# Kernel optimization log

Hardware: AMD Instinct MI355X
Metric: run time of the kernel (lower is better)

The kernel has to match this reference:

```python
import jax, jax.numpy as jnp
import numpy as np

EPS = 1e-8  # torch CosineSimilarity default eps


def setup_inputs() -> dict:
    key = jax.random.key(0)
    ks = jax.random.split(key, 7)
    B, C, W, E, D = 64, 256, 256, 2048, 2048
    return {
        "x_img_dense": jax.random.normal(ks[0], (B, C, E), dtype=jnp.float32),
        "x_txt_dense": jax.random.normal(ks[1], (B, W, E), dtype=jnp.float32),
        "y_what_card_leader_choose": jax.random.normal(ks[2], (B, C), dtype=jnp.float32),
        "W_img1": jax.random.normal(ks[3], (D, E), dtype=jnp.float32) * 0.02,
        "b_img1": jax.random.normal(ks[4], (D,), dtype=jnp.float32) * 0.02,
        "W_words1": jax.random.normal(ks[5], (D, E), dtype=jnp.float32) * 0.02,
        "b_words1": jax.random.normal(ks[6], (D,), dtype=jnp.float32) * 0.02,
    }


def reference(x_img_dense, x_txt_dense, y_what_card_leader_choose,
              W_img1, b_img1, W_words1, b_words1):
    # Default path: img_layer=True, words_layer=True, comb_layer=False,
    # same_img_words_layer=False, gumbel=False, inference=False.
    xi = jnp.einsum('bce,de->bcd', x_img_dense, W_img1) + b_img1   # [B, C, D]
    xt = jnp.einsum('bwe,de->bwd', x_txt_dense, W_words1) + b_words1  # [B, W, D]

    # gather leader card embedding per batch element
    idx = jnp.argmax(y_what_card_leader_choose, axis=1)            # [B]
    leader = jnp.take_along_axis(xi, idx[:, None, None], axis=1)[:, 0, :]  # [B, D]

    # cosine similarity (dim=2 in torch): leader broadcast over words axis
    dot = jnp.einsum('bd,bwd->bw', leader, xt)                     # [B, W]
    denom = jnp.linalg.norm(leader, axis=-1, keepdims=True) * jnp.linalg.norm(xt, axis=-1)
    logits = dot / jnp.maximum(denom, EPS)                         # [B, W]

    # module returns softmax of `logits` (logits_final is dead code)
    return jax.nn.softmax(logits, axis=1)
```

## Files before the change

kernel.cpp:

```cpp
#include <hip/hip_runtime.h>
#include <hip/hip_bf16.h>
#include <stdint.h>

typedef unsigned short u16;
typedef __bf16 bf16x8 __attribute__((ext_vector_type(8)));
typedef float  f32x4  __attribute__((ext_vector_type(4)));
typedef float  fvec4  __attribute__((ext_vector_type(4)));

constexpr int NB = 64;
constexpr int NC = 256;
constexpr int NW = 256;
constexpr int NE = 2048;
constexpr int ND = 2048;
constexpr int MROWS = NB * NW;

constexpr int BM = 128, BN = 128, BK = 64;
constexpr int KSPLIT = 4;
constexpr int KSLICE = NE / KSPLIT;
constexpr int NSLOT = 16;

constexpr size_t OFF_IDX  = 0;
constexpr size_t OFF_PART = 256;
constexpr size_t OFF_DOTP = 2097408;
constexpr size_t OFF_SSQP = 3145984;
constexpr size_t OFF_WW   = 4194560;
constexpr size_t OFF_XT   = 12583168;
constexpr size_t NEED_FULL = OFF_XT + 67108864ull;

__device__ __forceinline__ u16 f2bf(float f) {
    uint32_t u = __float_as_uint(f);
    u += 0x7fffu + ((u >> 16) & 1u);
    return (u16)(u >> 16);
}

__global__ void k_conv_argmax(const float* __restrict__ a, u16* __restrict__ da, int n4a,
                              const float* __restrict__ b, u16* __restrict__ db, int n4b,
                              const float* __restrict__ y, int* __restrict__ idx) {
    if (blockIdx.x == 0) {
        int t = threadIdx.x;
        int row = t >> 2, c = t & 3;
        float best = -3.4e38f; int bi = 0;
        for (int k = 0; k < 64; ++k) {
            int j = c + k * 4;
            float v = y[row * NC + j];
            if (v > best) { best = v; bi = j; }
        }
        #pragma unroll
        for (int off = 1; off <= 2; off <<= 1) {
            float ov = __shfl_xor(best, off, 64);
            int   oi = __shfl_xor(bi,   off, 64);
            if (ov > best || (ov == best && oi < bi)) { best = ov; bi = oi; }
        }
        if (c == 0) idx[row] = bi;
        return;
    }
    int i0 = (blockIdx.x - 1) * blockDim.x + threadIdx.x;
    int stride = (gridDim.x - 1) * blockDim.x;
    int n4 = n4a + n4b;
    for (int i = i0; i < n4; i += stride) {
        const fvec4* sp; ushort4* dp; int j;
        if (i < n4a) { sp = (const fvec4*)a; dp = (ushort4*)da; j = i; }
        else         { sp = (const fvec4*)b; dp = (ushort4*)db; j = i - n4a; }
        fvec4 v = __builtin_nontemporal_load(&sp[j]);
        ushort4 o = { f2bf(v.x), f2bf(v.y), f2bf(v.z), f2bf(v.w) };
        dp[j] = o;
    }
}

__global__ __launch_bounds__(256) void k_gemm0(
    const float* __restrict__ ximg, const int* __restrict__ idx,
    const float* __restrict__ Wimg, float* __restrict__ part)
{
    __shared__ __align__(16) u16 sA[BM * BK];
    __shared__ __align__(16) u16 sB[BN * BK];
    __shared__ int s_idx[64];

    const int t  = threadIdx.x;
    const int l  = t & 63;
    const int wv = t >> 6;
    const int wm = wv >> 1, wn = wv & 1;

    const int nt = blockIdx.x >> 2, ks = blockIdx.x & 3;
    const int n0 = nt * BN;
    const int kbase = ks * KSLICE;

    if (t < 64) s_idx[t] = idx[t];

    f32x4 acc[4][4];
    #pragma unroll
    for (int i = 0; i < 4; ++i)
        #pragma unroll
        for (int j = 0; j < 4; ++j) acc[i][j] = (f32x4){0.f, 0.f, 0.f, 0.f};

    const int lr = l >> 3, lp = l & 7;

    for (int k0 = kbase; k0 < kbase + KSLICE; k0 += BK) {
        __syncthreads();
        #pragma unroll
        for (int i = 0; i < 4; ++i) {
            int r = wv * 32 + i * 8 + lr;
            int g = lp ^ (r & 7);
            if (r < 64) {
                const float* src = ximg + ((size_t)r * NC + s_idx[r]) * NE + k0 + g * 8;
                float4 v0 = *(const float4*)src;
                float4 v1 = *(const float4*)(src + 4);
                uint4 ov;
                ov.x = (uint32_t)f2bf(v0.x) | ((uint32_t)f2bf(v0.y) << 16);
                ov.y = (uint32_t)f2bf(v0.z) | ((uint32_t)f2bf(v0.w) << 16);
                ov.z = (uint32_t)f2bf(v1.x) | ((uint32_t)f2bf(v1.y) << 16);
                ov.w = (uint32_t)f2bf(v1.z) | ((uint32_t)f2bf(v1.w) << 16);
                *(uint4*)&sA[r * BK + lp * 8] = ov;
            } else {
                *(uint4*)&sA[r * BK + lp * 8] = (uint4){0, 0, 0, 0};
            }
        }
        #pragma unroll
        for (int i = 0; i < 4; ++i) {
            int r = wv * 32 + i * 8 + lr;
            int g = lp ^ (r & 7);
            const float* src = Wimg + (size_t)(n0 + r) * NE + kbase + (k0 - kbase) + g * 8;
            src = Wimg + (size_t)(n0 + r) * NE + k0 + g * 8;
            float4 v0 = *(const float4*)src;
            float4 v1 = *(const float4*)(src + 4);
            uint4 ov;
            ov.x = (uint32_t)f2bf(v0.x) | ((uint32_t)f2bf(v0.y) << 16);
            ov.y = (uint32_t)f2bf(v0.z) | ((uint32_t)f2bf(v0.w) << 16);
            ov.z = (uint32_t)f2bf(v1.x) | ((uint32_t)f2bf(v1.y) << 16);
            ov.w = (uint32_t)f2bf(v1.z) | ((uint32_t)f2bf(v1.w) << 16);
            *(uint4*)&sB[r * BK + lp * 8] = ov;
        }
        __syncthreads();

        #pragma unroll
        for (int kk = 0; kk < 2; ++kk) {
            bf16x8 af[4], bfr[4];
            #pragma unroll
            for (int mi = 0; mi < 4; ++mi) {
                int ra = wm * 64 + mi * 16 + (l & 15);
                int g  = kk * 4 + (l >> 4);
                int p  = g ^ (ra & 7);
                af[mi] = *(const bf16x8*)&sA[ra * BK + p * 8];
            }
            #pragma unroll
            for (int nj = 0; nj < 4; ++nj) {
                int rb = wn * 64 + nj * 16 + (l & 15);
                int g  = kk * 4 + (l >> 4);
                int p  = g ^ (rb & 7);
                bfr[nj] = *(const bf16x8*)&sB[rb * BK + p * 8];
            }
            #pragma unroll
            for (int mi = 0; mi < 4; ++mi)
                #pragma unroll
                for (int nj = 0; nj < 4; ++nj)
                    acc[mi][nj] = __builtin_amdgcn_mfma_f32_16x16x32_bf16(
                        af[mi], bfr[nj], acc[mi][nj], 0, 0, 0);
        }
    }

    if (wm == 0) {
        const int quad = l >> 4, lc = l & 15;
        #pragma unroll
        for (int mi = 0; mi < 4; ++mi)
            #pragma unroll
            for (int r = 0; r < 4; ++r) {
                int m = mi * 16 + quad * 4 + r;
                #pragma unroll
                for (int nj = 0; nj < 4; ++nj) {
                    int n = n0 + wn * 64 + nj * 16 + lc;
                    part[((size_t)ks * NB + m) * ND + n] = acc[mi][nj][r];
                }
            }
    }
}

template<bool ABF, bool BBF>
__global__ __launch_bounds__(256) void k_gemm1(
    const void* __restrict__ Av, const void* __restrict__ Bv,
    const float* __restrict__ bwrd, const float* __restrict__ bimg,
    const float* __restrict__ part,
    float* __restrict__ dotp, float* __restrict__ ssqp)
{
    __shared__ __align__(16) u16 sA[BM * BK];
    __shared__ __align__(16) u16 sB[BN * BK];

    const int t  = threadIdx.x;
    const int l  = t & 63;
    const int wv = t >> 6;
    const int wm = wv >> 1, wn = wv & 1;

    const int mt = blockIdx.x >> 4;
    const int nt = blockIdx.x & 15;
    const int m0 = mt * BM, n0 = nt * BN;

    f32x4 acc[4][4];
    #pragma unroll
    for (int i = 0; i < 4; ++i)
        #pragma unroll
        for (int jj = 0; jj < 4; ++jj) acc[i][jj] = (f32x4){0.f, 0.f, 0.f, 0.f};

    const int lr = l >> 3, lp = l & 7;

    for (int k0 = 0; k0 < NE; k0 += BK) {
        __syncthreads();
        #pragma unroll
        for (int i = 0; i < 4; ++i) {
            int r = wv * 32 + i * 8 + lr;
            int g = lp ^ (r & 7);
            if (ABF) {
                const u16* src = (const u16*)Av + (size_t)(m0 + r) * NE + k0 + g * 8;
                __builtin_amdgcn_global_load_lds(
                    (const __attribute__((address_space(1))) void*)src,
                    (__attribute__((address_space(3))) void*)&sA[(wv * 32 + i * 8) * BK],
                    16, 0, 0);
            } else {
                const float* src = (const float*)Av + (size_t)(m0 + r) * NE + k0 + g * 8;
                float4 v0 = *(const float4*)src;
                float4 v1 = *(const float4*)(src + 4);
                uint4 ov;
                ov.x = (uint32_t)f2bf(v0.x) | ((uint32_t)f2bf(v0.y) << 16);
                ov.y = (uint32_t)f2bf(v0.z) | ((uint32_t)f2bf(v0.w) << 16);
                ov.z = (uint32_t)f2bf(v1.x) | ((uint32_t)f2bf(v1.y) << 16);
                ov.w = (uint32_t)f2bf(v1.z) | ((uint32_t)f2bf(v1.w) << 16);
                *(uint4*)&sA[r * BK + lp * 8] = ov;
            }
        }
        #pragma unroll
        for (int i = 0; i < 4; ++i) {
            int r = wv * 32 + i * 8 + lr;
            int g = lp ^ (r & 7);
            if (BBF) {
                const u16* src = (const u16*)Bv + (size_t)(n0 + r) * NE + k0 + g * 8;
                __builtin_amdgcn_global_load_lds(
                    (const __attribute__((address_space(1))) void*)src,
                    (__attribute__((address_space(3))) void*)&sB[(wv * 32 + i * 8) * BK],
                    16, 0, 0);
            } else {
                const float* src = (const float*)Bv + (size_t)(n0 + r) * NE + k0 + g * 8;
                float4 v0 = *(const float4*)src;
                float4 v1 = *(const float4*)(src + 4);
                uint4 ov;
                ov.x = (uint32_t)f2bf(v0.x) | ((uint32_t)f2bf(v0.y) << 16);
                ov.y = (uint32_t)f2bf(v0.z) | ((uint32_t)f2bf(v0.w) << 16);
                ov.z = (uint32_t)f2bf(v1.x) | ((uint32_t)f2bf(v1.y) << 16);
                ov.w = (uint32_t)f2bf(v1.z) | ((uint32_t)f2bf(v1.w) << 16);
                *(uint4*)&sB[r * BK + lp * 8] = ov;
            }
        }
        __syncthreads();

        #pragma unroll
        for (int kk = 0; kk < 2; ++kk) {
            bf16x8 af[4], bfr[4];
            #pragma unroll
            for (int mi = 0; mi < 4; ++mi) {
                int ra = wm * 64 + mi * 16 + (l & 15);
                int g  = kk * 4 + (l >> 4);
                int p  = g ^ (ra & 7);
                af[mi] = *(const bf16x8*)&sA[ra * BK + p * 8];
            }
            #pragma unroll
            for (int nj = 0; nj < 4; ++nj) {
                int rb = wn * 64 + nj * 16 + (l & 15);
                int g  = kk * 4 + (l >> 4);
                int p  = g ^ (rb & 7);
                bfr[nj] = *(const bf16x8*)&sB[rb * BK + p * 8];
            }
            #pragma unroll
            for (int mi = 0; mi < 4; ++mi)
                #pragma unroll
                for (int nj = 0; nj < 4; ++nj)
                    acc[mi][nj] = __builtin_amdgcn_mfma_f32_16x16x32_bf16(
                        af[mi], bfr[nj], acc[mi][nj], 0, 0, 0);
        }
    }

    const int quad = l >> 4, lc = l & 15;
    const int bidx = m0 >> 8;
    float bia[4], ldr[4];
    #pragma unroll
    for (int nj = 0; nj < 4; ++nj) {
        int n = n0 + wn * 64 + nj * 16 + lc;
        bia[nj] = bwrd[n];
        float ld = bimg[n];
        #pragma unroll
        for (int ks = 0; ks < KSPLIT; ++ks)
            ld += part[((size_t)ks * NB + bidx) * ND + n];
        ldr[nj] = ld;
    }
    __syncthreads();
    float* sRed = (float*)sA;
    #pragma unroll
    for (int mi = 0; mi < 4; ++mi) {
        #pragma unroll
        for (int r = 0; r < 4; ++r) {
            float pd = 0.f, ps = 0.f;
            #pragma unroll
            for (int nj = 0; nj < 4; ++nj) {
                float v = acc[mi][nj][r] + bia[nj];
                pd += ldr[nj] * v;
                ps += v * v;
            }
            #pragma unroll
            for (int off = 1; off <= 8; off <<= 1) {
                pd += __shfl_xor(pd, off, 64);
                ps += __shfl_xor(ps, off, 64);
            }
            if (lc == 0) {
                int lm = mi * 16 + quad * 4 + r;
                sRed[(wm * 2 + wn) * 64 + lm]       = pd;
                sRed[256 + (wm * 2 + wn) * 64 + lm] = ps;
            }
        }
    }
    __syncthreads();
    if (t < 128) {
        int wmm = t >> 6, lm = t & 63;
        int m = m0 + wmm * 64 + lm;
        dotp[(size_t)nt * MROWS + m] =
            sRed[(wmm * 2 + 0) * 64 + lm] + sRed[(wmm * 2 + 1) * 64 + lm];
        ssqp[(size_t)nt * MROWS + m] =
            sRed[256 + (wmm * 2 + 0) * 64 + lm] + sRed[256 + (wmm * 2 + 1) * 64 + lm];
    }
}

__global__ void k_final(const float* __restrict__ part, const float* __restrict__ bimg,
                        const float* __restrict__ dotp, const float* __restrict__ ssqp,
                        float* __restrict__ out) {
    int b = blockIdx.x, t = threadIdx.x;
    __shared__ float rsum[4], redm[4], reds[4];
    float s2 = 0.f;
    #pragma unroll
    for (int i = 0; i < 8; ++i) {
        int d = i * 256 + t;
        float ld = bimg[d];
        #pragma unroll
        for (int ks = 0; ks < KSPLIT; ++ks)
            ld += part[((size_t)ks * NB + b) * ND + d];
        s2 += ld * ld;
    }
    for (int off = 1; off < 64; off <<= 1) s2 += __shfl_xor(s2, off, 64);
    if ((t & 63) == 0) rsum[t >> 6] = s2;
    __syncthreads();
    float ln2 = rsum[0] + rsum[1] + rsum[2] + rsum[3];

    int m = b * NW + t;
    float dt = 0.f, sq = 0.f;
    #pragma unroll
    for (int s = 0; s < NSLOT; ++s) {
        dt += dotp[(size_t)s * MROWS + m];
        sq += ssqp[(size_t)s * MROWS + m];
    }
    float dn = sqrtf(ln2) * sqrtf(sq);
    float lg = dt / fmaxf(dn, 1e-8f);
    float mx = lg;
    for (int off = 1; off < 64; off <<= 1) mx = fmaxf(mx, __shfl_xor(mx, off, 64));
    int wvi = t >> 6;
    if ((t & 63) == 0) redm[wvi] = mx;
    __syncthreads();
    mx = fmaxf(fmaxf(redm[0], redm[1]), fmaxf(redm[2], redm[3]));
    float e = __expf(lg - mx);
    float s = e;
    for (int off = 1; off < 64; off <<= 1) s += __shfl_xor(s, off, 64);
    if ((t & 63) == 0) reds[wvi] = s;
    __syncthreads();
    s = reds[0] + reds[1] + reds[2] + reds[3];
    out[m] = e / s;
}

extern "C" void kernel_launch(void* const* d_in, const int* in_sizes, int n_in,
                              void* d_out, int out_size, void* d_ws, size_t ws_size,
                              hipStream_t stream) {
    const float* ximg = (const float*)d_in[0];
    const float* xtxt = (const float*)d_in[1];
    const float* y    = (const float*)d_in[2];
    const float* Wimg = (const float*)d_in[3];
    const float* bimg = (const float*)d_in[4];
    const float* Wwrd = (const float*)d_in[5];
    const float* bwrd = (const float*)d_in[6];
    float* out = (float*)d_out;

    char* ws = (char*)d_ws;
    int*   idx  = (int*)(ws + OFF_IDX);
    float* part = (float*)(ws + OFF_PART);
    float* dotp = (float*)(ws + OFF_DOTP);
    float* ssqp = (float*)(ws + OFF_SSQP);
    u16*   WWb  = (u16*)(ws + OFF_WW);
    u16*   XTb  = (u16*)(ws + OFF_XT);

    const bool preconv = ws_size >= NEED_FULL;

    if (preconv) {
        k_conv_argmax<<<4097, 256, 0, stream>>>(Wwrd, WWb, ND * NE / 4,
                                                xtxt, XTb, MROWS * NE / 4, y, idx);
        k_gemm0<<<(ND / BN) * KSPLIT, 256, 0, stream>>>(ximg, idx, Wimg, part);
        k_gemm1<true, true><<<(MROWS / BM) * (ND / BN), 256, 0, stream>>>(
            XTb, WWb, bwrd, bimg, part, dotp, ssqp);
    } else {
        k_conv_argmax<<<1, 256, 0, stream>>>(nullptr, nullptr, 0,
                                             nullptr, nullptr, 0, y, idx);
        k_gemm0<<<(ND / BN) * KSPLIT, 256, 0, stream>>>(ximg, idx, Wimg, part);
        k_gemm1<false, false><<<(MROWS / BM) * (ND / BN), 256, 0, stream>>>(
            xtxt, Wwrd, bwrd, bimg, part, dotp, ssqp);
    }
    k_final<<<NB, 256, 0, stream>>>(part, bimg, dotp, ssqp, out);
}
```

Before: 464.4 us.

## Replace bf16 text GEMM with 256x256-tile, 8-wave, double-buffered interleaved pipeline

Adds a new kernel for the main text-by-word-weight GEMM on the pre-converted bf16 path. It uses 256x256 tiles with 512 threads and double-buffered LDS, and issues async global-to-LDS loads for the next tiles between MFMA phases under raised wave priority. Explicit vmcnt waits and barriers replace the per-k-tile syncthreads. The larger tiles halve the partial-slot count that k_final must reduce. In exchange it uses more LDS and registers per block, and the hand-tuned waitcnt schedule is fragile.

```diff
diff --git a/kernel.cpp b/kernel.cpp
--- a/kernel.cpp
+++ b/kernel.cpp
@@ -17,7 +17,11 @@
 constexpr int BM = 128, BN = 128, BK = 64;
 constexpr int KSPLIT = 4;
 constexpr int KSLICE = NE / KSPLIT;
-constexpr int NSLOT = 16;
+
+constexpr int BM2 = 256, BN2 = 256;
+constexpr int NT_K = NE / BK;
+constexpr int NSLOT2 = ND / BN2;
+constexpr int NSLOT1 = ND / BN;
 
 constexpr size_t OFF_IDX  = 0;
 constexpr size_t OFF_PART = 256;
@@ -118,8 +122,7 @@
         for (int i = 0; i < 4; ++i) {
             int r = wv * 32 + i * 8 + lr;
             int g = lp ^ (r & 7);
-            const float* src = Wimg + (size_t)(n0 + r) * NE + kbase + (k0 - kbase) + g * 8;
-            src = Wimg + (size_t)(n0 + r) * NE + k0 + g * 8;
+            const float* src = Wimg + (size_t)(n0 + r) * NE + k0 + g * 8;
             float4 v0 = *(const float4*)src;
             float4 v1 = *(const float4*)(src + 4);
             uint4 ov;
@@ -173,9 +176,167 @@
     }
 }
 
-template<bool ABF, bool BBF>
-__global__ __launch_bounds__(256) void k_gemm1(
-    const void* __restrict__ Av, const void* __restrict__ Bv,
+#define GLD(sp, dp) __builtin_amdgcn_global_load_lds( \
+    (const __attribute__((address_space(1))) void*)(sp), \
+    (__attribute__((address_space(3))) void*)(dp), 16, 0, 0)
+
+#define STAGE_HALF(srcbase, h, kt, dstarr) do { \
+    const u16* _s = (srcbase) + (size_t)(h) * 128 * NE + (size_t)(kt) * BK; \
+    u16* _d = &(dstarr)[(h) * 8192 + dst0]; \
+    GLD(_s, _d); \
+    GLD(_s + (size_t)64 * NE, _d + 4096); \
+} while (0)
+
+#define TILE(S, tt) do { \
+    const u16* slA = &lds[S][0][0]; \
+    const u16* slB = &lds[S][1][0]; \
+    bf16x8 a[8][2], b[4][2]; \
+     \
+    _Pragma("unroll") for (int mi = 0; mi < 4; ++mi) a[mi][0] = *(const bf16x8*)&slA[arow + mi * 1024 + pk0]; \
+    _Pragma("unroll") for (int nj = 0; nj < 4; ++nj) b[nj][0] = *(const bf16x8*)&slB[brow + nj * 1024 + pk0]; \
+    _Pragma("unroll") for (int mi = 0; mi < 4; ++mi) a[mi][1] = *(const bf16x8*)&slA[arow + mi * 1024 + pk1]; \
+    if ((tt) + 1 < NT_K) STAGE_HALF(Bsrc, 0, (tt) + 1, lds[(S) ^ 1][1]); \
+    __builtin_amdgcn_s_setprio(1); \
+    _Pragma("unroll") for (int mi = 0; mi < 4; ++mi) \
+        _Pragma("unroll") for (int nj = 0; nj < 4; ++nj) \
+            acc[mi][nj] = __builtin_amdgcn_mfma_f32_16x16x32_bf16(a[mi][0], b[nj][0], acc[mi][nj], 0, 0, 0); \
+    __builtin_amdgcn_s_setprio(0); \
+     \
+    _Pragma("unroll") for (int mi = 4; mi < 8; ++mi) a[mi][0] = *(const bf16x8*)&slA[arow + mi * 1024 + pk0]; \
+    _Pragma("unroll") for (int nj = 0; nj < 4; ++nj) b[nj][1] = *(const bf16x8*)&slB[brow + nj * 1024 + pk1]; \
+    _Pragma("unroll") for (int mi = 4; mi < 8; ++mi) a[mi][1] = *(const bf16x8*)&slA[arow + mi * 1024 + pk1]; \
+    if ((tt) + 1 < NT_K) STAGE_HALF(Bsrc, 1, (tt) + 1, lds[(S) ^ 1][1]); \
+    __builtin_amdgcn_s_setprio(1); \
+    _Pragma("unroll") for (int mi = 0; mi < 4; ++mi) \
+        _Pragma("unroll") for (int nj = 0; nj < 4; ++nj) \
+            acc[mi][nj] = __builtin_amdgcn_mfma_f32_16x16x32_bf16(a[mi][1], b[nj][1], acc[mi][nj], 0, 0, 0); \
+    __builtin_amdgcn_s_setprio(0); \
+    asm volatile("s_waitcnt lgkmcnt(0)" ::: "memory"); \
+    __builtin_amdgcn_s_barrier(); \
+     \
+    if ((tt) + 2 < NT_K) STAGE_HALF(Asrc, 0, (tt) + 2, lds[S][0]); \
+    __builtin_amdgcn_s_setprio(1); \
+    _Pragma("unroll") for (int mi = 4; mi < 8; ++mi) \
+        _Pragma("unroll") for (int nj = 0; nj < 4; ++nj) \
+            acc[mi][nj] = __builtin_amdgcn_mfma_f32_16x16x32_bf16(a[mi][0], b[nj][0], acc[mi][nj], 0, 0, 0); \
+    __builtin_amdgcn_s_setprio(0); \
+     \
+    if ((tt) + 2 < NT_K) STAGE_HALF(Asrc, 1, (tt) + 2, lds[S][0]); \
+    __builtin_amdgcn_s_setprio(1); \
+    _Pragma("unroll") for (int mi = 4; mi < 8; ++mi) \
+        _Pragma("unroll") for (int nj = 0; nj < 4; ++nj) \
+            acc[mi][nj] = __builtin_amdgcn_mfma_f32_16x16x32_bf16(a[mi][1], b[nj][1], acc[mi][nj], 0, 0, 0); \
+    __builtin_amdgcn_s_setprio(0); \
+    if ((tt) < NT_K - 2) { asm volatile("s_waitcnt vmcnt(4)" ::: "memory"); } \
+    else                 { asm volatile("s_waitcnt vmcnt(0)" ::: "memory"); } \
+    __builtin_amdgcn_s_barrier(); \
+} while (0)
+
+__global__ __launch_bounds__(512, 2) void k_gemm1_8ph(
+    const u16* __restrict__ A, const u16* __restrict__ B,
+    const float* __restrict__ bwrd, const float* __restrict__ bimg,
+    const float* __restrict__ part,
+    float* __restrict__ dotp, float* __restrict__ ssqp)
+{
+    __shared__ __align__(16) u16 lds[2][2][16384];
+
+    const int t  = threadIdx.x;
+    const int l  = t & 63;
+    const int wv = t >> 6;
+    const int wm = wv >> 2;
+    const int wn = wv & 3;
+
+    const int mt = blockIdx.x >> 3;
+    const int nt = blockIdx.x & 7;
+    const int m0 = mt * BM2, n0 = nt * BN2;
+
+    const int r0 = t >> 3;
+    const int ge = ((t & 7) ^ (r0 & 7)) * 8;
+    const u16* Asrc = A + (size_t)(m0 + r0) * NE + ge;
+    const u16* Bsrc = B + (size_t)(n0 + r0) * NE + ge;
+    const int dst0 = wv * 512;
+
+    const int lc16 = l & 15, khi = l >> 4, lx = l & 7;
+    const int pk0 = (khi ^ lx) * 8;
+    const int pk1 = ((4 + khi) ^ lx) * 8;
+    const int arow = (wm * 128 + lc16) * 64;
+    const int brow = (wn * 64 + lc16) * 64;
+
+    f32x4 acc[8][4];
+    #pragma unroll
+    for (int i = 0; i < 8; ++i)
+        #pragma unroll
+        for (int j = 0; j < 4; ++j) acc[i][j] = (f32x4){0.f, 0.f, 0.f, 0.f};
+
+    STAGE_HALF(Asrc, 0, 0, lds[0][0]);
+    STAGE_HALF(Asrc, 1, 0, lds[0][0]);
+    STAGE_HALF(Bsrc, 0, 0, lds[0][1]);
+    STAGE_HALF(Bsrc, 1, 0, lds[0][1]);
+    STAGE_HALF(Asrc, 0, 1, lds[1][0]);
+    STAGE_HALF(Asrc, 1, 1, lds[1][0]);
+    asm volatile("s_waitcnt vmcnt(4)" ::: "memory");
+    __builtin_amdgcn_s_barrier();
+
+    #pragma unroll 1
+    for (int it = 0; it < NT_K / 2; ++it) {
+        const int tt0 = it * 2;
+        TILE(0, tt0);
+        TILE(1, tt0 + 1);
+    }
+
+    const int quad = l >> 4, lc = l & 15;
+    float bia[4], ldr[4];
+    #pragma unroll
+    for (int nj = 0; nj < 4; ++nj) {
+        int n = n0 + wn * 64 + nj * 16 + lc;
+        bia[nj] = bwrd[n];
+        float ld = bimg[n];
+        #pragma unroll
+        for (int ks = 0; ks < KSPLIT; ++ks)
+            ld += part[((size_t)ks * NB + mt) * ND + n];
+        ldr[nj] = ld;
+    }
+    __syncthreads();
+    float* sRed = (float*)&lds[0][0][0];
+    #pragma unroll
+    for (int mi = 0; mi < 8; ++mi) {
+        #pragma unroll
+        for (int r = 0; r < 4; ++r) {
+            float pd = 0.f, ps = 0.f;
+            #pragma unroll
+            for (int nj = 0; nj < 4; ++nj) {
+                float v = acc[mi][nj][r] + bia[nj];
+                pd += ldr[nj] * v;
+                ps += v * v;
+            }
+            #pragma unroll
+            for (int off = 1; off <= 8; off <<= 1) {
+                pd += __shfl_xor(pd, off, 64);
+                ps += __shfl_xor(ps, off, 64);
+            }
+            if (lc == 0) {
+                int row = mi * 16 + quad * 4 + r;
+                sRed[(wm * 128 + row) * 4 + wn]        = pd;
+                sRed[1024 + (wm * 128 + row) * 4 + wn] = ps;
+            }
+        }
+    }
+    __syncthreads();
+    if (t < 256) {
+        int m = m0 + t;
+        const fvec4* s4 = (const fvec4*)sRed;
+        fvec4 vd = s4[t], vs = s4[256 + t];
+        dotp[(size_t)nt * MROWS + m] = vd.x + vd.y + vd.z + vd.w;
+        ssqp[(size_t)nt * MROWS + m] = vs.x + vs.y + vs.z + vs.w;
+    }
+}
+
+#undef TILE
+#undef STAGE_HALF
+#undef GLD
+
+__global__ __launch_bounds__(256) void k_gemm1_f32(
+    const float* __restrict__ Av, const float* __restrict__ Bv,
     const float* __restrict__ bwrd, const float* __restrict__ bimg,
     const float* __restrict__ part,
     float* __restrict__ dotp, float* __restrict__ ssqp)
@@ -206,45 +367,29 @@
         for (int i = 0; i < 4; ++i) {
             int r = wv * 32 + i * 8 + lr;
             int g = lp ^ (r & 7);
-            if (ABF) {
-                const u16* src = (const u16*)Av + (size_t)(m0 + r) * NE + k0 + g * 8;
-                __builtin_amdgcn_global_load_lds(
-                    (const __attribute__((address_space(1))) void*)src,
-                    (__attribute__((address_space(3))) void*)&sA[(wv * 32 + i * 8) * BK],
-                    16, 0, 0);
-            } else {
-                const float* src = (const float*)Av + (size_t)(m0 + r) * NE + k0 + g * 8;
-                float4 v0 = *(const float4*)src;
-                float4 v1 = *(const float4*)(src + 4);
-                uint4 ov;
-                ov.x = (uint32_t)f2bf(v0.x) | ((uint32_t)f2bf(v0.y) << 16);
-                ov.y = (uint32_t)f2bf(v0.z) | ((uint32_t)f2bf(v0.w) << 16);
-                ov.z = (uint32_t)f2bf(v1.x) | ((uint32_t)f2bf(v1.y) << 16);
-                ov.w = (uint32_t)f2bf(v1.z) | ((uint32_t)f2bf(v1.w) << 16);
-                *(uint4*)&sA[r * BK + lp * 8] = ov;
-            }
+            const float* src = Av + (size_t)(m0 + r) * NE + k0 + g * 8;
+            float4 v0 = *(const float4*)src;
+            float4 v1 = *(const float4*)(src + 4);
+            uint4 ov;
+            ov.x = (uint32_t)f2bf(v0.x) | ((uint32_t)f2bf(v0.y) << 16);
+            ov.y = (uint32_t)f2bf(v0.z) | ((uint32_t)f2bf(v0.w) << 16);
+            ov.z = (uint32_t)f2bf(v1.x) | ((uint32_t)f2bf(v1.y) << 16);
+            ov.w = (uint32_t)f2bf(v1.z) | ((uint32_t)f2bf(v1.w) << 16);
+            *(uint4*)&sA[r * BK + lp * 8] = ov;
         }
         #pragma unroll
         for (int i = 0; i < 4; ++i) {
             int r = wv * 32 + i * 8 + lr;
             int g = lp ^ (r & 7);
-            if (BBF) {
-                const u16* src = (const u16*)Bv + (size_t)(n0 + r) * NE + k0 + g * 8;
-                __builtin_amdgcn_global_load_lds(
-                    (const __attribute__((address_space(1))) void*)src,
-                    (__attribute__((address_space(3))) void*)&sB[(wv * 32 + i * 8) * BK],
-                    16, 0, 0);
-            } else {
-                const float* src = (const float*)Bv + (size_t)(n0 + r) * NE + k0 + g * 8;
-                float4 v0 = *(const float4*)src;
-                float4 v1 = *(const float4*)(src + 4);
-                uint4 ov;
-                ov.x = (uint32_t)f2bf(v0.x) | ((uint32_t)f2bf(v0.y) << 16);
-                ov.y = (uint32_t)f2bf(v0.z) | ((uint32_t)f2bf(v0.w) << 16);
-                ov.z = (uint32_t)f2bf(v1.x) | ((uint32_t)f2bf(v1.y) << 16);
-                ov.w = (uint32_t)f2bf(v1.z) | ((uint32_t)f2bf(v1.w) << 16);
-                *(uint4*)&sB[r * BK + lp * 8] = ov;
-            }
+            const float* src = Bv + (size_t)(n0 + r) * NE + k0 + g * 8;
+            float4 v0 = *(const float4*)src;
+            float4 v1 = *(const float4*)(src + 4);
+            uint4 ov;
+            ov.x = (uint32_t)f2bf(v0.x) | ((uint32_t)f2bf(v0.y) << 16);
+            ov.y = (uint32_t)f2bf(v0.z) | ((uint32_t)f2bf(v0.w) << 16);
+            ov.z = (uint32_t)f2bf(v1.x) | ((uint32_t)f2bf(v1.y) << 16);
+            ov.w = (uint32_t)f2bf(v1.z) | ((uint32_t)f2bf(v1.w) << 16);
+            *(uint4*)&sB[r * BK + lp * 8] = ov;
         }
         __syncthreads();
 
@@ -325,7 +470,7 @@
 
 __global__ void k_final(const float* __restrict__ part, const float* __restrict__ bimg,
                         const float* __restrict__ dotp, const float* __restrict__ ssqp,
-                        float* __restrict__ out) {
+                        float* __restrict__ out, int nslot) {
     int b = blockIdx.x, t = threadIdx.x;
     __shared__ float rsum[4], redm[4], reds[4];
     float s2 = 0.f;
@@ -345,8 +490,7 @@
 
     int m = b * NW + t;
     float dt = 0.f, sq = 0.f;
-    #pragma unroll
-    for (int s = 0; s < NSLOT; ++s) {
+    for (int s = 0; s < nslot; ++s) {
         dt += dotp[(size_t)s * MROWS + m];
         sq += ssqp[(size_t)s * MROWS + m];
     }
@@ -393,14 +537,15 @@
         k_conv_argmax<<<4097, 256, 0, stream>>>(Wwrd, WWb, ND * NE / 4,
                                                 xtxt, XTb, MROWS * NE / 4, y, idx);
         k_gemm0<<<(ND / BN) * KSPLIT, 256, 0, stream>>>(ximg, idx, Wimg, part);
-        k_gemm1<true, true><<<(MROWS / BM) * (ND / BN), 256, 0, stream>>>(
+        k_gemm1_8ph<<<(MROWS / BM2) * (ND / BN2), 512, 0, stream>>>(
             XTb, WWb, bwrd, bimg, part, dotp, ssqp);
+        k_final<<<NB, 256, 0, stream>>>(part, bimg, dotp, ssqp, out, NSLOT2);
     } else {
         k_conv_argmax<<<1, 256, 0, stream>>>(nullptr, nullptr, 0,
                                              nullptr, nullptr, 0, y, idx);
         k_gemm0<<<(ND / BN) * KSPLIT, 256, 0, stream>>>(ximg, idx, Wimg, part);
-        k_gemm1<false, false><<<(MROWS / BM) * (ND / BN), 256, 0, stream>>>(
+        k_gemm1_f32<<<(MROWS / BM) * (ND / BN), 256, 0, stream>>>(
             xtxt, Wwrd, bwrd, bimg, part, dotp, ssqp);
-    }
-    k_final<<<NB, 256, 0, stream>>>(part, bimg, dotp, ssqp, out);
-}
+        k_final<<<NB, 256, 0, stream>>>(part, bimg, dotp, ssqp, out, NSLOT1);
+    }
+}
```

After: 469.4 us. No clear change (+1.1%).
